# Kernel optimization log

Measured on AMD Instinct MI355X. Metric: run time of the kernel, lower is better.

## Reference

```python
import jax, jax.numpy as jnp
import numpy as np

BLUR = 5e-5
P = 2
EPS = BLUR ** P          # geomloss: temperature eps = blur**p
N_ITERS = 30             # fixed log-domain Sinkhorn sweeps


def _cost(x, y):
    # geomloss p=2 cost: C_ij = |x_i - y_j|^2 / 2   ([N,D],[M,D] -> [N,M])
    x2 = jnp.sum(x * x, axis=-1)[:, None]
    y2 = jnp.sum(y * y, axis=-1)[None, :]
    return 0.5 * (x2 + y2 - 2.0 * (x @ y.T))


def _softmin(C, pot, log_w):
    # f_i = -eps * logsumexp_j( log_w_j + (pot_j - C_ij)/eps )
    return -EPS * jax.nn.logsumexp(log_w[None, :] + (pot[None, :] - C) / EPS, axis=1)


def _ot_potentials(C, loga, logb):
    def step(carry, _):
        f, g = carry
        f = _softmin(C, g, logb)
        g = _softmin(C.T, f, loga)
        return (f, g), None
    f0 = jnp.zeros((C.shape[0],), C.dtype)
    g0 = jnp.zeros((C.shape[1],), C.dtype)
    (f, g), _ = jax.lax.scan(jax.checkpoint(step), (f0, g0), None, length=N_ITERS)
    return f, g


def _self_potential(C, log_w):
    # symmetric OT(x,x): averaged fixed-point updates of a single potential
    def step(p, _):
        return 0.5 * (p + _softmin(C, p, log_w)), None
    p0 = jnp.zeros((C.shape[0],), C.dtype)
    p, _ = jax.lax.scan(jax.checkpoint(step), p0, None, length=N_ITERS)
    return p


def _sinkhorn_divergence(px, py):
    # px: [N,D], py: [M,D] point clouds with uniform weights
    N, M = px.shape[0], py.shape[0]
    loga = jnp.full((N,), -np.log(N), px.dtype)
    logb = jnp.full((M,), -np.log(M), py.dtype)
    Cxy = _cost(px, py)
    Cxx = _cost(px, px)
    Cyy = _cost(py, py)
    f, g = _ot_potentials(Cxy, loga, logb)
    pxx = _self_potential(Cxx, loga)
    pyy = _self_potential(Cyy, logb)
    # S = OT(x,y) - 0.5*OT(x,x) - 0.5*OT(y,y); uniform weights -> means
    return jnp.mean(f) + jnp.mean(g) - jnp.mean(pxx) - jnp.mean(pyy)


def setup_inputs() -> dict:
    key = jax.random.key(0)
    kx, ky = jax.random.split(key)
    x = jax.random.normal(kx, (4, 1500, 300), dtype=jnp.float32)
    y = jax.random.normal(ky, (4, 1500, 300), dtype=jnp.float32)
    return {"x": x, "y": y}


def reference(x, y):
    B = x.shape[0]

    def per_pair(xb, yb):
        # square, then normalize each receiver trace (column) to unit mass
        px = xb ** 2
        px = px / jnp.sum(px, axis=0, keepdims=True)
        py = yb ** 2
        py = py / jnp.sum(py, axis=0, keepdims=True)
        return _sinkhorn_divergence(px, py)

    losses = jax.vmap(per_pair)(x, y)  # [B]
    # original code's inner `for i in range(x.shape[0])` adds the same
    # scalar B times per pair -> total = B * sum_b loss_b
    return jnp.asarray(B, x.dtype) * jnp.sum(losses)
```

## Files before the change

kernel.cpp:

```cpp
#include <hip/hip_runtime.h>
#include <hip/hip_fp16.h>

#define NP 1500
#define DD 300
#define DP 320
#define VSZ 1536
#define NB 4
#define TILE 16384
#define TSZ (1536*1536)
#define OTB 16
#define NCH 125
#define KADD 1.8283051e-8f
#define PADVAL (-60000.0f)
#define SCALE 256.0f
#define SCALE2INV (1.0f/65536.0f)
#define FTHR 1e-8f

typedef _Float16 f16x8 __attribute__((ext_vector_type(8)));
typedef float f32x4 __attribute__((ext_vector_type(4)));

__device__ __forceinline__ unsigned fkey(float f){
    unsigned b = __float_as_uint(f);
    return (b & 0x80000000u) ? ~b : (b | 0x80000000u);
}
__device__ __forceinline__ float funkey(unsigned k){
    unsigned b = (k & 0x80000000u) ? (k & 0x7FFFFFFFu) : ~k;
    return __uint_as_float(b);
}

__global__ __launch_bounds__(256) void k_colsum_p1(const float* __restrict__ x, const float* __restrict__ y,
                                                   float* __restrict__ partial,
                                                   int* __restrict__ barsflags,
                                                   unsigned* __restrict__ cmin){
    int rc = blockIdx.x, b = blockIdx.y, src = blockIdx.z;
    int tid = threadIdx.x;
    if (rc == NCH){
        int idx = (b*2 + src)*256 + tid;
        if (idx < 1536 + 2 + 8) barsflags[idx] = 0;
        for (int k = idx; k < 4*3*1536; k += 2048) cmin[k] = 0xFFFFFFFFu;
        return;
    }
    const float* in = (src ? y : x) + ((size_t)b*NP + rc*12)*DD;
    float s0 = 0.f, s1 = 0.f;
    #pragma unroll
    for (int r = 0; r < 12; ++r){
        float v0 = in[r*DD + tid];
        s0 = fmaf(v0, v0, s0);
        if (tid < 44){
            float v1 = in[r*DD + 256 + tid];
            s1 = fmaf(v1, v1, s1);
        }
    }
    float* po = partial + (((size_t)rc*NB + b)*2 + src)*DD;
    po[tid] = s0;
    if (tid < 44) po[256 + tid] = s1;
}

__global__ void k_colsum_p2(const float* __restrict__ partial,
                            float* __restrict__ csx, float* __restrict__ csy){
    int idx = blockIdx.x*256 + threadIdx.x;
    if (idx >= NB*2*DD) return;
    int c = idx % DD; int t = idx / DD; int src = t & 1; int b = t >> 1;
    float s = 0.f;
    for (int rc = 0; rc < NCH; ++rc)
        s += partial[(((size_t)rc*NB + b)*2 + src)*DD + c];
    (src ? csy : csx)[b*DD + c] = s;
}

__global__ __launch_bounds__(256) void k_normrow(const float* __restrict__ x, const float* __restrict__ y,
        const float* __restrict__ csx, const float* __restrict__ csy,
        __half* __restrict__ pxh, __half* __restrict__ pyh,
        float* __restrict__ xnrm, float* __restrict__ uvv, float* __restrict__ ynrm,
        unsigned* __restrict__ cmin){
    int gw = ((int)blockIdx.x*256 + threadIdx.x) >> 6;
    int lane = threadIdx.x & 63;
    int src = (gw >= NB*NP) ? 1 : 0;
    int rem = gw - src*NB*NP;
    int b = rem / NP, i = rem - b*NP;
    const float* in = (src ? y : x) + ((size_t)b*NP + i)*DD;
    const float* cs = (src ? csy : csx) + b*DD;
    __half* oph = (src ? pyh : pxh) + ((size_t)b*NP + i)*DP;
    float s = 0.f;
    #pragma unroll
    for (int it = 0; it < 5; ++it){
        int c = lane + it*64;
        float vu = 0.f, hv = 0.f;
        if (c < DD){
            float u = in[c];
            vu = u*u / cs[c];
            hv = vu * SCALE;
        }
        oph[c] = __float2half(hv);
        s = fmaf(vu, vu, s);
    }
    #pragma unroll
    for (int o2 = 1; o2 < 64; o2 <<= 1) s += __shfl_xor(s, o2, 64);
    if (lane == 0){
        float val = 0.5f * s;
        int o = b*VSZ + i;
        if (src){
            uvv[o] = val; ynrm[o] = val;
            cmin[(b*3 + 2)*1536 + i] = fkey(-(val + KADD));
        } else {
            xnrm[o] = val;
        }
    }
}

__global__ __launch_bounds__(1024) void k_gemm_mfma(const __half* __restrict__ pxh,
                                                    const __half* __restrict__ pyh,
                                                    __half* __restrict__ P){
    int n = (int)blockIdx.x;
    int xcd = n & 7;
    int b = xcd & 3;
    int t = (xcd >> 2)*72 + (n >> 3);
    int bx = t / 12, by = t - bx*12;
    const __half* A = pxh + (size_t)b*NP*DP;
    const __half* B = pyh + (size_t)b*NP*DP;

    __shared__ __align__(16) char smem[128*136*2];
    char* ldsA = smem;
    char* ldsB = smem + 16384;
    __half* ldsO = (__half*)smem;

    int tid = threadIdx.x;
    int row0 = bx*128, col0 = by*128;
    int lane = tid & 63;
    int w = tid >> 6;
    int wm = (w >> 2)*32, wn = (w & 3)*32;
    int g8 = tid & 7, rw = tid >> 3;
    int lr = lane & 15, cq = lane >> 4;

    f32x4 acc[2][2];
    #pragma unroll
    for (int mi = 0; mi < 2; ++mi)
        #pragma unroll
        for (int ni = 0; ni < 2; ++ni)
            acc[mi][ni] = (f32x4){0.f, 0.f, 0.f, 0.f};

    uint4 va, vb;
    {
        int ar = row0 + rw; if (ar > NP-1) ar = NP-1;
        int br = col0 + rw; if (br > NP-1) br = NP-1;
        va = *(const uint4*)(A + (size_t)ar*DP + g8*8);
        vb = *(const uint4*)(B + (size_t)br*DP + g8*8);
    }
    #pragma unroll
    for (int ks = 0; ks < 5; ++ks){
        if (ks) __syncthreads();
        {
            int pc = g8 ^ (rw & 7);
            *(uint4*)(ldsA + rw*128 + pc*16) = va;
            *(uint4*)(ldsB + rw*128 + pc*16) = vb;
        }
        __syncthreads();
        if (ks < 4){
            int k0 = (ks + 1)*64;
            int ar = row0 + rw; if (ar > NP-1) ar = NP-1;
            int br = col0 + rw; if (br > NP-1) br = NP-1;
            va = *(const uint4*)(A + (size_t)ar*DP + k0 + g8*8);
            vb = *(const uint4*)(B + (size_t)br*DP + k0 + g8*8);
        }
        f16x8 av[2][2], bv[2][2];
        #pragma unroll
        for (int ksl = 0; ksl < 2; ++ksl){
            int lc = ksl*4 + cq;
            int pc = (lc ^ (lr & 7))*16;
            #pragma unroll
            for (int mi = 0; mi < 2; ++mi)
                av[ksl][mi] = *(const f16x8*)(ldsA + (wm + mi*16 + lr)*128 + pc);
            #pragma unroll
            for (int ni = 0; ni < 2; ++ni)
                bv[ksl][ni] = *(const f16x8*)(ldsB + (wn + ni*16 + lr)*128 + pc);
        }
        #pragma unroll
        for (int ksl = 0; ksl < 2; ++ksl)
            #pragma unroll
            for (int mi = 0; mi < 2; ++mi)
                #pragma unroll
                for (int ni = 0; ni < 2; ++ni)
                    acc[mi][ni] = __builtin_amdgcn_mfma_f32_16x16x32_f16(av[ksl][mi], bv[ksl][ni], acc[mi][ni], 0, 0, 0);
    }

    int cqe = lane >> 4;
    __syncthreads();
    #pragma unroll
    for (int mi = 0; mi < 2; ++mi)
        #pragma unroll
        for (int ni = 0; ni < 2; ++ni){
            int lcol = wn + ni*16 + lr;
            bool colok = (col0 + lcol) < NP;
            #pragma unroll
            for (int v = 0; v < 4; ++v){
                int lrow = wm + mi*16 + cqe*4 + v;
                bool rowok = (row0 + lrow) < NP;
                ldsO[lrow*136 + lcol] = __float2half((colok && rowok) ? acc[mi][ni][v]*SCALE2INV : PADVAL);
            }
        }
    __syncthreads();
    {
        __half* tileD = P + (size_t)(b*4 + 0)*TSZ + ((size_t)bx*12 + by)*TILE;
        #pragma unroll
        for (int it = 0; it < 2; ++it){
            int e = it*1024 + tid;
            int r = e >> 4, q = e & 15;
            *(uint4*)(tileD + r*128 + q*8) = *(const uint4*)(ldsO + r*136 + q*8);
        }
    }
}

__device__ __forceinline__ void groupbar(int* slot, int gsz){
    __syncthreads();
    if (threadIdx.x == 0){
        __hip_atomic_fetch_add(slot, 1, __ATOMIC_RELEASE, __HIP_MEMORY_SCOPE_AGENT);
        while (__hip_atomic_load(slot, __ATOMIC_ACQUIRE, __HIP_MEMORY_SCOPE_AGENT) < gsz)
            __builtin_amdgcn_s_sleep(1);
    }
    __syncthreads();
}

#define ROWPTR(PK, i) ((PK) + (size_t)((i) >> 7)*12*TILE + (size_t)((i) & 127)*128)

__global__ __launch_bounds__(1024, 1) void k_sink(const __half* __restrict__ P,
        float* __restrict__ fs, float* __restrict__ uvv,
        const float* __restrict__ xnrm, const float* __restrict__ ynrm,
        int* __restrict__ bars, int* __restrict__ flags,
        unsigned* __restrict__ cmin,
        int* __restrict__ done, double* __restrict__ partS,
        float* __restrict__ out){
    int tid = threadIdx.x;
    int lane = tid & 63;
    int wid = tid >> 6;
    int blk = (int)blockIdx.x;
    __shared__ int s_ch;
    __shared__ unsigned lmin[1536];
    __shared__ double red[1024];

    int b = blk / OTB, lb = blk - b*OTB;
    int gw = lb*16 + wid;
    const int NWV = OTB*16;
    int* gbarp  = bars + b*64;
    int* gflagp = flags + b*64;
    const __half* P0 = P + (size_t)(b*4 + 0)*TSZ;
    float* fsb = fs + b*VSZ;
    float* uvb = uvv + b*VSZ;
    unsigned* cm = cmin + b*3*1536;

    int colb[3];
    #pragma unroll
    for (int it = 0; it < 3; ++it){
        int c = lane + it*64;
        colb[it] = ((c >> 4) << 7) + ((c & 15) << 3);
    }

    int lastT = 0;
    for (int t = 0; t < 30; ++t){
        unsigned* rdbuf = cm + ((t + 2) % 3)*1536;
        unsigned* wrbuf = cm + (t % 3)*1536;
        unsigned* rsbuf = cm + ((t + 1) % 3)*1536;
        if (tid == 0) s_ch = 0;
        for (int idx = tid; idx < 1536; idx += 1024) lmin[idx] = 0xFFFFFFFFu;
        float Au[3][8];
        #pragma unroll
        for (int it = 0; it < 3; ++it){
            uint4 k0 = *(const uint4*)(rdbuf + colb[it]);
            uint4 k1 = *(const uint4*)(rdbuf + colb[it] + 4);
            unsigned kk[8] = {k0.x, k0.y, k0.z, k0.w, k1.x, k1.y, k1.z, k1.w};
            #pragma unroll
            for (int e = 0; e < 8; ++e){
                int col = colb[it] + e;
                Au[it][e] = (col < NP) ? (-(funkey(kk[e]) + KADD)) : 3.0e38f;
            }
        }
        __syncthreads();
        float amin[3][8];
        #pragma unroll
        for (int it = 0; it < 3; ++it)
            #pragma unroll
            for (int e = 0; e < 8; ++e) amin[it][e] = 3.0e38f;
        int ch = 0;
        for (int i = gw; i < NP; i += NWV){
            const __half* rowb = ROWPTR(P0, i);
            uint4 pk[3];
            #pragma unroll
            for (int it = 0; it < 3; ++it){
                int c = lane + it*64, tt = c >> 4, q = c & 15;
                pk[it] = *(const uint4*)(rowb + (size_t)tt*TILE + q*8);
            }
            float cf[3][8];
            float m = 3.0e38f;
            #pragma unroll
            for (int it = 0; it < 3; ++it){
                float2 c0 = __half22float2(*(const __half2*)&pk[it].x);
                float2 c1 = __half22float2(*(const __half2*)&pk[it].y);
                float2 c2 = __half22float2(*(const __half2*)&pk[it].z);
                float2 c3 = __half22float2(*(const __half2*)&pk[it].w);
                cf[it][0] = c0.x; cf[it][1] = c0.y; cf[it][2] = c1.x; cf[it][3] = c1.y;
                cf[it][4] = c2.x; cf[it][5] = c2.y; cf[it][6] = c3.x; cf[it][7] = c3.y;
                #pragma unroll
                for (int e = 0; e < 8; ++e) m = fminf(m, Au[it][e] - cf[it][e]);
            }
            #pragma unroll
            for (int o = 1; o < 64; o <<= 1) m = fminf(m, __shfl_xor(m, o, 64));
            float nv = -(m + KADD);
            if (lane == 0){
                if (fabsf(nv - fsb[i]) > FTHR) ch = 1;
                fsb[i] = nv;
            }
            #pragma unroll
            for (int it = 0; it < 3; ++it)
                #pragma unroll
                for (int e = 0; e < 8; ++e)
                    amin[it][e] = fminf(amin[it][e], nv - cf[it][e]);
        }
        if (ch) s_ch = 1;
        #pragma unroll
        for (int it = 0; it < 3; ++it)
            #pragma unroll
            for (int e = 0; e < 8; ++e)
                atomicMin(&lmin[colb[it] + e], fkey(amin[it][e]));
        __syncthreads();
        for (int idx = tid; idx < 1536; idx += 1024)
            atomicMin(&wrbuf[idx], lmin[idx]);
        if (tid < 96) rsbuf[lb*96 + tid] = 0xFFFFFFFFu;
        if (tid == 0 && s_ch) atomicOr(&gflagp[t], 1);
        groupbar(&gbarp[t], OTB);
        lastT = t;
        int fA = __hip_atomic_load(&gflagp[t], __ATOMIC_RELAXED, __HIP_MEMORY_SCOPE_AGENT);
        if (fA == 0) break;
    }
    unsigned* fin = cm + (lastT % 3)*1536;
    for (int j = tid; j < NP; j += 1024)
        uvb[j] = -(funkey(fin[j]) + KADD);

    if (lb == 0){
        const float* xb = xnrm + b*VSZ;
        const float* yb = ynrm + b*VSZ;
        double s = 0.0;
        for (int i = tid; i < NP; i += 1024)
            s += (double)xb[i] + (double)yb[i] - (double)fsb[i] - (double)uvb[i];
        __syncthreads();
        red[tid] = s; __syncthreads();
        for (int w2 = 512; w2 > 0; w2 >>= 1){
            if (tid < w2) red[tid] += red[tid + w2];
            __syncthreads();
        }
        if (tid == 0){
            partS[b] = red[0];
            int old = __hip_atomic_fetch_add(done, 1, __ATOMIC_ACQ_REL, __HIP_MEMORY_SCOPE_AGENT);
            if (old == 3)
                out[0] = (float)((partS[0] + partS[1] + partS[2] + partS[3]) * (4.0/1500.0));
        }
    }
}

extern "C" void kernel_launch(void* const* d_in, const int* in_sizes, int n_in,
                              void* d_out, int out_size, void* d_ws, size_t ws_size,
                              hipStream_t stream) {
    const float* x = (const float*)d_in[0];
    const float* y = (const float*)d_in[1];
    float* out = (float*)d_out;

    __half* pxh = (__half*)d_ws;
    __half* pyh = pxh + (size_t)NB*NP*DP;
    float* csx = (float*)(pyh + (size_t)NB*NP*DP);
    float* csy = csx + NB*DD;
    float* fs  = csy + NB*DD;
    float* uv  = fs + NB*VSZ;
    float* xnrm = uv + NB*VSZ;
    float* ynrm = xnrm + NB*VSZ;
    int* bars  = (int*)(ynrm + NB*VSZ);
    int* flags = bars + 12*64;
    int* done  = flags + 12*64;
    double* partS = (double*)(done + 2);
    unsigned* cmin = (unsigned*)(partS + 4);
    float* partial = (float*)(cmin + 4*3*1536);
    float* smallEnd = partial + (size_t)NCH*NB*2*DD;
    size_t pOff = (((size_t)((char*)smallEnd - (char*)d_ws)) + 255) & ~(size_t)255;
    __half* P = (__half*)((char*)d_ws + pOff);

    k_colsum_p1<<<dim3(NCH + 1, NB, 2), 256, 0, stream>>>(x, y, partial, bars, cmin);
    k_colsum_p2<<<10, 256, 0, stream>>>(partial, csx, csy);

    k_normrow<<<3000, 256, 0, stream>>>(x, y, csx, csy, pxh, pyh, xnrm, uv, ynrm, cmin);

    k_gemm_mfma<<<576, 1024, 0, stream>>>(pxh, pyh, P);

    k_sink<<<4*OTB, 1024, 0, stream>>>(P, fs, uv, xnrm, ynrm, bars, flags, cmin, done, partS, out);
}
```

Before: 63.99 us.

## Double OT blocks per batch and unroll row loop with hoisted loads

```diff
diff --git a/kernel.cpp b/kernel.cpp
--- a/kernel.cpp
+++ b/kernel.cpp
@@ -8,7 +8,7 @@
 #define NB 4
 #define TILE 16384
 #define TSZ (1536*1536)
-#define OTB 16
+#define OTB 32
 #define NCH 125
 #define KADD 1.8283051e-8f
 #define PADVAL (-60000.0f)
@@ -246,11 +246,23 @@
     float* uvb = uvv + b*VSZ;
     unsigned* cm = cmin + b*3*1536;
 
+    int i0 = gw, i1 = gw + NWV, i2 = gw + 2*NWV;
+    bool has1 = (i1 < NP), has2 = (i2 < NP);
+    const __half* rb0 = ROWPTR(P0, i0);
+    const __half* rb1 = has1 ? ROWPTR(P0, i1) : rb0;
+    const __half* rb2 = has2 ? ROWPTR(P0, i2) : rb0;
+
     int colb[3];
     #pragma unroll
     for (int it = 0; it < 3; ++it){
         int c = lane + it*64;
         colb[it] = ((c >> 4) << 7) + ((c & 15) << 3);
+    }
+    int rowoff[3];
+    #pragma unroll
+    for (int it = 0; it < 3; ++it){
+        int c = lane + it*64, tt = c >> 4, q = c & 15;
+        rowoff[it] = tt*TILE + q*8;
     }
 
     int lastT = 0;
@@ -272,6 +284,13 @@
                 Au[it][e] = (col < NP) ? (-(funkey(kk[e]) + KADD)) : 3.0e38f;
             }
         }
+        uint4 pk0[3], pk1[3], pk2[3];
+        #pragma unroll
+        for (int it = 0; it < 3; ++it) pk0[it] = *(const uint4*)(rb0 + rowoff[it]);
+        #pragma unroll
+        for (int it = 0; it < 3; ++it) pk1[it] = *(const uint4*)(rb1 + rowoff[it]);
+        #pragma unroll
+        for (int it = 0; it < 3; ++it) pk2[it] = *(const uint4*)(rb2 + rowoff[it]);
         __syncthreads();
         float amin[3][8];
         #pragma unroll
@@ -279,22 +298,15 @@
             #pragma unroll
             for (int e = 0; e < 8; ++e) amin[it][e] = 3.0e38f;
         int ch = 0;
-        for (int i = gw; i < NP; i += NWV){
-            const __half* rowb = ROWPTR(P0, i);
-            uint4 pk[3];
-            #pragma unroll
-            for (int it = 0; it < 3; ++it){
-                int c = lane + it*64, tt = c >> 4, q = c & 15;
-                pk[it] = *(const uint4*)(rowb + (size_t)tt*TILE + q*8);
-            }
+        {
             float cf[3][8];
             float m = 3.0e38f;
             #pragma unroll
             for (int it = 0; it < 3; ++it){
-                float2 c0 = __half22float2(*(const __half2*)&pk[it].x);
-                float2 c1 = __half22float2(*(const __half2*)&pk[it].y);
-                float2 c2 = __half22float2(*(const __half2*)&pk[it].z);
-                float2 c3 = __half22float2(*(const __half2*)&pk[it].w);
+                float2 c0 = __half22float2(*(const __half2*)&pk0[it].x);
+                float2 c1 = __half22float2(*(const __half2*)&pk0[it].y);
+                float2 c2 = __half22float2(*(const __half2*)&pk0[it].z);
+                float2 c3 = __half22float2(*(const __half2*)&pk0[it].w);
                 cf[it][0] = c0.x; cf[it][1] = c0.y; cf[it][2] = c1.x; cf[it][3] = c1.y;
                 cf[it][4] = c2.x; cf[it][5] = c2.y; cf[it][6] = c3.x; cf[it][7] = c3.y;
                 #pragma unroll
@@ -304,8 +316,62 @@
             for (int o = 1; o < 64; o <<= 1) m = fminf(m, __shfl_xor(m, o, 64));
             float nv = -(m + KADD);
             if (lane == 0){
-                if (fabsf(nv - fsb[i]) > FTHR) ch = 1;
-                fsb[i] = nv;
+                if (fabsf(nv - fsb[i0]) > FTHR) ch = 1;
+                fsb[i0] = nv;
+            }
+            #pragma unroll
+            for (int it = 0; it < 3; ++it)
+                #pragma unroll
+                for (int e = 0; e < 8; ++e)
+                    amin[it][e] = fminf(amin[it][e], nv - cf[it][e]);
+        }
+        if (has1){
+            float cf[3][8];
+            float m = 3.0e38f;
+            #pragma unroll
+            for (int it = 0; it < 3; ++it){
+                float2 c0 = __half22float2(*(const __half2*)&pk1[it].x);
+                float2 c1 = __half22float2(*(const __half2*)&pk1[it].y);
+                float2 c2 = __half22float2(*(const __half2*)&pk1[it].z);
+                float2 c3 = __half22float2(*(const __half2*)&pk1[it].w);
+                cf[it][0] = c0.x; cf[it][1] = c0.y; cf[it][2] = c1.x; cf[it][3] = c1.y;
+                cf[it][4] = c2.x; cf[it][5] = c2.y; cf[it][6] = c3.x; cf[it][7] = c3.y;
+                #pragma unroll
+                for (int e = 0; e < 8; ++e) m = fminf(m, Au[it][e] - cf[it][e]);
+            }
+            #pragma unroll
+            for (int o = 1; o < 64; o <<= 1) m = fminf(m, __shfl_xor(m, o, 64));
+            float nv = -(m + KADD);
+            if (lane == 0){
+                if (fabsf(nv - fsb[i1]) > FTHR) ch = 1;
+                fsb[i1] = nv;
+            }
+            #pragma unroll
+            for (int it = 0; it < 3; ++it)
+                #pragma unroll
+                for (int e = 0; e < 8; ++e)
+                    amin[it][e] = fminf(amin[it][e], nv - cf[it][e]);
+        }
+        if (has2){
+            float cf[3][8];
+            float m = 3.0e38f;
+            #pragma unroll
+            for (int it = 0; it < 3; ++it){
+                float2 c0 = __half22float2(*(const __half2*)&pk2[it].x);
+                float2 c1 = __half22float2(*(const __half2*)&pk2[it].y);
+                float2 c2 = __half22float2(*(const __half2*)&pk2[it].z);
+                float2 c3 = __half22float2(*(const __half2*)&pk2[it].w);
+                cf[it][0] = c0.x; cf[it][1] = c0.y; cf[it][2] = c1.x; cf[it][3] = c1.y;
+                cf[it][4] = c2.x; cf[it][5] = c2.y; cf[it][6] = c3.x; cf[it][7] = c3.y;
+                #pragma unroll
+                for (int e = 0; e < 8; ++e) m = fminf(m, Au[it][e] - cf[it][e]);
+            }
+            #pragma unroll
+            for (int o = 1; o < 64; o <<= 1) m = fminf(m, __shfl_xor(m, o, 64));
+            float nv = -(m + KADD);
+            if (lane == 0){
+                if (fabsf(nv - fsb[i2]) > FTHR) ch = 1;
+                fsb[i2] = nv;
             }
             #pragma unroll
             for (int it = 0; it < 3; ++it)
@@ -322,7 +388,7 @@
         __syncthreads();
         for (int idx = tid; idx < 1536; idx += 1024)
             atomicMin(&wrbuf[idx], lmin[idx]);
-        if (tid < 96) rsbuf[lb*96 + tid] = 0xFFFFFFFFu;
+        if (tid < 48) rsbuf[lb*48 + tid] = 0xFFFFFFFFu;
         if (tid == 0 && s_ch) atomicOr(&gflagp[t], 1);
         groupbar(&gbarp[t], OTB);
         lastT = t;
```

Result: slower. 67.79 us (+5.9%).
